# Kernel tuning notes

Measured on AMD Instinct MI355X. Metric: run time of the kernel, lower is better.

## Reference

```python
import jax, jax.numpy as jnp
import numpy as np

EPS = 1e-5

def _add_self_loops(edge_index, n):
    loop = jnp.arange(n, dtype=edge_index.dtype)
    return jnp.concatenate([edge_index, jnp.stack([loop, loop])], axis=1)

def _gcn_norm(row, col, n, dtype):
    # degree of target nodes (with self loops, unit edge weights)
    deg = jax.ops.segment_sum(jnp.ones(row.shape[0], dtype=dtype), col, num_segments=n)
    dinv = jnp.where(deg > 0, deg ** -0.5, 0.0).astype(dtype)
    return dinv[row] * dinv[col]  # [E]

def _propagate(xw, row, col, ew, n):
    # gather -> scale -> scatter-add
    msgs = ew[:, None] * xw[row]          # [E, C]
    return jax.ops.segment_sum(msgs, col, num_segments=n)  # [N, C]

def _batchnorm(x, gamma, beta):
    mu = jnp.mean(x, axis=0)
    var = jnp.var(x, axis=0)
    return (x - mu) * jax.lax.rsqrt(var + EPS) * gamma + beta

def setup_inputs() -> dict:
    key = jax.random.key(0)
    ks = jax.random.split(key, 10)
    N, C_in, C_h, C_out, E = 50000, 128, 128, 1, 600000
    x = jax.random.normal(ks[0], (N, C_in), dtype=jnp.float32)
    edge_index = jax.random.randint(ks[1], (2, E), 0, N, dtype=jnp.int64)
    s = 1.0 / np.sqrt(C_in)
    return {
        "x": x,
        "edge_index": edge_index,
        "gcn_w": jax.random.uniform(ks[2], (C_in, C_h), jnp.float32, -s, s),
        "gcn_b": jnp.zeros((C_h,), jnp.float32),
        "bn1_g": jnp.ones((C_h,), jnp.float32),
        "bn1_b": jnp.zeros((C_h,), jnp.float32),
        "dcn_w": jax.random.uniform(ks[3], (C_h, C_h), jnp.float32, -s, s),
        "dcn_b": jnp.zeros((C_h,), jnp.float32),
        "bn3_g": jnp.ones((C_h,), jnp.float32),
        "bn3_b": jnp.zeros((C_h,), jnp.float32),
        "out_w": jax.random.uniform(ks[4], (2 * C_h, C_out), jnp.float32, -s, s),
        "out_b": jnp.zeros((C_out,), jnp.float32),
    }

def reference(x, edge_index, gcn_w, gcn_b, bn1_g, bn1_b, dcn_w, dcn_b, bn3_g, bn3_b, out_w, out_b):
    n = x.shape[0]
    ei = _add_self_loops(edge_index, n)
    row, col = ei[0], ei[1]
    ew = _gcn_norm(row, col, n, x.dtype)

    # GCNConv: lin -> normalized aggregate -> bias
    h = _propagate(x @ gcn_w, row, col, ew, n) + gcn_b
    h = _batchnorm(h, bn1_g, bn1_b)

    # DegGNNConv: lin -> normalized aggregate -> elementwise gate with input -> bias
    out = _propagate(h @ dcn_w, row, col, ew, n)
    out = out * h + dcn_b
    out = _batchnorm(out, bn3_g, bn3_b)
    # dropout is identity in eval mode

    xc = jnp.concatenate([h, out], axis=-1)  # [N, 2*C_h]
    return xc @ out_w + out_b
```

## Files before the change

### kernel.cpp

```cpp
#include <hip/hip_runtime.h>
#include <hip/hip_bf16.h>
#include <cstdint>


typedef __attribute__((ext_vector_type(8))) short bf16x8;
typedef __attribute__((ext_vector_type(4))) float f32x4;

__device__ __forceinline__ ushort f2bf(float f) {
    union { float f; unsigned u; } c; c.f = f;
    unsigned u = c.u;
    return (ushort)((u + 0x7fffu + ((u >> 16) & 1u)) >> 16);
}
__device__ __forceinline__ unsigned pack2bf(float a, float b) {
    return (unsigned)f2bf(a) | ((unsigned)f2bf(b) << 16);
}
__device__ __forceinline__ float bflo(unsigned u) {
    union { unsigned i; float f; } c; c.i = u << 16; return c.f;
}
__device__ __forceinline__ float bfhi(unsigned u) {
    union { unsigned i; float f; } c; c.i = u & 0xffff0000u; return c.f;
}

__global__ void zero_kernel(uint4* __restrict__ p, int nwords) {
    int i = blockIdx.x * blockDim.x + threadIdx.x;
    if (i < nwords) p[i] = (uint4){0u, 0u, 0u, 0u};
}

__global__ void convert_kernel(const void* __restrict__ ei, int E,
                               int* __restrict__ count) {
    const int* e32 = (const int*)ei;
    bool is64 = ((e32[1] | e32[3] | e32[5] | e32[7]) == 0);
    int stride = gridDim.x * blockDim.x;
    for (int e = blockIdx.x * blockDim.x + threadIdx.x; e < E; e += stride) {
        int c = is64 ? (int)((const long long*)ei)[E + e] : e32[E + e];
        atomicAdd(&count[c], 1);
    }
}

__global__ __launch_bounds__(256) void bsum_kernel(const int* __restrict__ count,
                                                   int* __restrict__ bsum, int n) {
    int t = threadIdx.x;
    int i0 = blockIdx.x * 1024 + t * 4;
    int s = 0;
    if (i0 + 4 <= n) {
        int4 v = *(const int4*)&count[i0];
        s = v.x + v.y + v.z + v.w;
    } else {
        for (int i = i0; i < n; i++) s += count[i];
    }
    __shared__ int ls[256];
    ls[t] = s;
    __syncthreads();
    for (int off = 128; off > 0; off >>= 1) {
        if (t < off) ls[t] += ls[t + off];
        __syncthreads();
    }
    if (t == 0) bsum[blockIdx.x] = ls[0];
}

__global__ void scanb_kernel(int* __restrict__ bsum, int nb) {
    __shared__ int sm[1024];
    int t = threadIdx.x;
    int v = (t < nb) ? bsum[t] : 0;
    sm[t] = v;
    __syncthreads();
    for (int off = 1; off < 1024; off <<= 1) {
        int a = (t >= off) ? sm[t - off] : 0;
        __syncthreads();
        sm[t] += a;
        __syncthreads();
    }
    if (t < nb) bsum[t] = sm[t] - v;
}

__global__ __launch_bounds__(256) void emit_kernel(const int* __restrict__ count,
                                                   const int* __restrict__ bbase,
                                                   int* __restrict__ base, int n) {
    int t = threadIdx.x;
    int i0 = blockIdx.x * 1024 + t * 4;
    int v[4];
    int s = 0;
    if (i0 + 4 <= n) {
        int4 q = *(const int4*)&count[i0];
        v[0] = q.x; v[1] = q.y; v[2] = q.z; v[3] = q.w;
        s = v[0] + v[1] + v[2] + v[3];
    } else {
        #pragma unroll
        for (int k = 0; k < 4; k++) {
            int i = i0 + k;
            v[k] = (i < n) ? count[i] : 0;
            s += v[k];
        }
    }
    __shared__ int sm[256];
    sm[t] = s;
    __syncthreads();
    for (int off = 1; off < 256; off <<= 1) {
        int a = (t >= off) ? sm[t - off] : 0;
        __syncthreads();
        sm[t] += a;
        __syncthreads();
    }
    int run = bbase[blockIdx.x] + sm[t] - s;
    #pragma unroll
    for (int k = 0; k < 4; k++) {
        int i = i0 + k;
        if (i < n) {
            base[i] = run;
            run += v[k];
        }
    }
}

__global__ void scatter_kernel(const void* __restrict__ ei, int E,
                               const int* __restrict__ base, int* __restrict__ cursor,
                               const int* __restrict__ count,
                               unsigned* __restrict__ esrc) {
    const int* e32 = (const int*)ei;
    bool is64 = ((e32[1] | e32[3] | e32[5] | e32[7]) == 0);
    int stride = gridDim.x * blockDim.x;
    for (int e = blockIdx.x * blockDim.x + threadIdx.x; e < E; e += stride) {
        int r, c;
        if (is64) {
            r = (int)((const long long*)ei)[e];
            c = (int)((const long long*)ei)[E + e];
        } else {
            r = e32[e];
            c = e32[E + e];
        }
        int pos = base[c] + atomicAdd(&cursor[c], 1);
        unsigned deg = (unsigned)count[r];
        esrc[pos] = (deg << 24) | ((unsigned)r << 6);
    }
}

__global__ void wtrans_kernel(const float* __restrict__ W1, ushort* __restrict__ WT1,
                              const float* __restrict__ W2, ushort* __restrict__ WT2) {
    int b = blockIdx.x;
    const float* W = (b < 64) ? W1 : W2;
    ushort* WT = (b < 64) ? WT1 : WT2;
    int t = (b & 63) * 256 + threadIdx.x;
    int c = t >> 7, k = t & 127;
    WT[t] = f2bf(W[k * 128 + c]);
}

__global__ __launch_bounds__(256) void gemm_mfma_kernel(const float* __restrict__ Xf,
                                                        const ushort* __restrict__ Xb,
                                                        const ushort* __restrict__ WT,
                                                        const float* __restrict__ ab,
                                                        ushort* __restrict__ Ybf, int n) {
    __shared__ ushort Wl[128 * 136];
    int t = threadIdx.x;
    for (int idx = t * 8; idx < 128 * 128; idx += 256 * 8) {
        int c = idx >> 7;
        int k = idx & 127;
        *(uint4*)&Wl[c * 136 + k] = *(const uint4*)&WT[idx];
    }
    __syncthreads();

    int wid = t >> 6;
    int lane = t & 63;
    int m0 = blockIdx.x * 64 + wid * 16;
    if (m0 >= n) return;
    int row = m0 + (lane & 15);
    int rc = row < n ? row : n - 1;
    int kg = (lane >> 4) * 8;

    f32x4 acc[8];
    #pragma unroll
    for (int i = 0; i < 8; i++) acc[i] = (f32x4){0.f, 0.f, 0.f, 0.f};

    #pragma unroll
    for (int ks = 0; ks < 4; ks++) {
        int k0 = ks * 32 + kg;
        bf16x8 a;
        if (Xb) {
            uint4 q = *(const uint4*)&Xb[(size_t)rc * 128 + k0];
            float f0 = bflo(q.x), f1 = bfhi(q.x), f2 = bflo(q.y), f3 = bfhi(q.y);
            float f4 = bflo(q.z), f5 = bfhi(q.z), f6 = bflo(q.w), f7 = bfhi(q.w);
            float4 alo = *(const float4*)&ab[k0];
            float4 ahi = *(const float4*)&ab[k0 + 4];
            float4 blo = *(const float4*)&ab[128 + k0];
            float4 bhi = *(const float4*)&ab[128 + k0 + 4];
            a[0] = (short)f2bf(alo.x * f0 + blo.x);
            a[1] = (short)f2bf(alo.y * f1 + blo.y);
            a[2] = (short)f2bf(alo.z * f2 + blo.z);
            a[3] = (short)f2bf(alo.w * f3 + blo.w);
            a[4] = (short)f2bf(ahi.x * f4 + bhi.x);
            a[5] = (short)f2bf(ahi.y * f5 + bhi.y);
            a[6] = (short)f2bf(ahi.z * f6 + bhi.z);
            a[7] = (short)f2bf(ahi.w * f7 + bhi.w);
        } else {
            const float* xr = &Xf[(size_t)rc * 128];
            float4 lo = *(const float4*)&xr[k0];
            float4 hi = *(const float4*)&xr[k0 + 4];
            a[0] = (short)f2bf(lo.x); a[1] = (short)f2bf(lo.y);
            a[2] = (short)f2bf(lo.z); a[3] = (short)f2bf(lo.w);
            a[4] = (short)f2bf(hi.x); a[5] = (short)f2bf(hi.y);
            a[6] = (short)f2bf(hi.z); a[7] = (short)f2bf(hi.w);
        }
        #pragma unroll
        for (int nt = 0; nt < 8; nt++) {
            int c = nt * 16 + (lane & 15);
            bf16x8 b = *(bf16x8*)&Wl[c * 136 + k0];
            acc[nt] = __builtin_amdgcn_mfma_f32_16x16x32_bf16(a, b, acc[nt], 0, 0, 0);
        }
    }

    int ro = m0 + (lane >> 4) * 4;
    int co = lane & 15;
    #pragma unroll
    for (int nt = 0; nt < 8; nt++) {
        #pragma unroll
        for (int i = 0; i < 4; i++) {
            int r = ro + i;
            if (r < n) Ybf[(size_t)r * 128 + nt * 16 + co] = f2bf(acc[nt][i]);
        }
    }
}

__global__ __launch_bounds__(256) void prop_kernel(const unsigned* __restrict__ XWb,
                            const int* __restrict__ base,
                            const int* __restrict__ count, const unsigned* __restrict__ esrc,
                            const unsigned* __restrict__ B1bf, const float* __restrict__ ab1,
                            unsigned* __restrict__ outbf,
                            float* __restrict__ psum, float* __restrict__ psq,
                            int n, int gate) {
    int wave = (int)((blockIdx.x * blockDim.x + threadIdx.x) >> 6);
    int lane = threadIdx.x & 63;
    int wid = threadIdx.x >> 6;
    float vx = 0.f, vy = 0.f;
    if (wave < n) {
        int b = base[wave];
        int cnt = count[wave];
        float din = rsqrtf((float)(cnt + 1));
        float accx = 0.f, accy = 0.f;
        unsigned vs = XWb[(size_t)wave * 64 + lane];
        int i = 0;
        for (; i + 8 <= cnt; i += 8) {
            unsigned p[8], v[8];
            #pragma unroll
            for (int j = 0; j < 8; j++) p[j] = esrc[b + i + j];
            #pragma unroll
            for (int j = 0; j < 8; j++)
                v[j] = XWb[(size_t)(p[j] & 0xFFFFFFu) + lane];
            #pragma unroll
            for (int j = 0; j < 8; j++) {
                float w = rsqrtf((float)((p[j] >> 24) + 1));
                accx += w * bflo(v[j]);
                accy += w * bfhi(v[j]);
            }
        }
        for (; i + 4 <= cnt; i += 4) {
            unsigned p[4], v[4];
            #pragma unroll
            for (int j = 0; j < 4; j++) p[j] = esrc[b + i + j];
            #pragma unroll
            for (int j = 0; j < 4; j++)
                v[j] = XWb[(size_t)(p[j] & 0xFFFFFFu) + lane];
            #pragma unroll
            for (int j = 0; j < 4; j++) {
                float w = rsqrtf((float)((p[j] >> 24) + 1));
                accx += w * bflo(v[j]);
                accy += w * bfhi(v[j]);
            }
        }
        for (; i < cnt; i++) {
            unsigned p = esrc[b + i];
            unsigned v = XWb[(size_t)(p & 0xFFFFFFu) + lane];
            float w = rsqrtf((float)((p >> 24) + 1));
            accx += w * bflo(v);
            accy += w * bfhi(v);
        }
        accx = din * (accx + din * bflo(vs));
        accy = din * (accy + din * bfhi(vs));
        if (gate) {
            int c0 = 2 * lane;
            unsigned b1 = B1bf[(size_t)wave * 64 + lane];
            float h0 = ab1[c0] * bflo(b1) + ab1[128 + c0];
            float h1 = ab1[c0 + 1] * bfhi(b1) + ab1[128 + c0 + 1];
            vx = accx * h0;
            vy = accy * h1;
        } else {
            vx = accx;
            vy = accy;
        }
        outbf[(size_t)wave * 64 + lane] = pack2bf(vx, vy);
    }
    __shared__ float4 sm[4][64];
    float4 st; st.x = vx; st.y = vx * vx; st.z = vy; st.w = vy * vy;
    sm[wid][lane] = st;
    __syncthreads();
    if (threadIdx.x < 64) {
        float4 a0 = sm[0][lane], a1 = sm[1][lane], a2 = sm[2][lane], a3 = sm[3][lane];
        float s0 = a0.x + a1.x + a2.x + a3.x;
        float q0 = a0.y + a1.y + a2.y + a3.y;
        float s1 = a0.z + a1.z + a2.z + a3.z;
        float q1 = a0.w + a1.w + a2.w + a3.w;
        int slot = (blockIdx.x & 63) * 128;
        int c0 = 2 * lane;
        atomicAdd(&psum[slot + c0], s0);
        atomicAdd(&psq[slot + c0], q0);
        atomicAdd(&psum[slot + c0 + 1], s1);
        atomicAdd(&psq[slot + c0 + 1], q1);
    }
}

__global__ void reduce_ab_kernel(const float* __restrict__ psum, const float* __restrict__ psq,
                                 const float* __restrict__ g, const float* __restrict__ beta,
                                 float* __restrict__ ab, int n) {
    int c = threadIdx.x;
    float s = 0.f, s2 = 0.f;
    for (int r = 0; r < 64; r++) {
        s += psum[r * 128 + c];
        s2 += psq[r * 128 + c];
    }
    float invn = 1.f / (float)n;
    float mu = s * invn;
    float var = s2 * invn - mu * mu;
    float a = g[c] * rsqrtf(var + 1e-5f);
    ab[c] = a;
    ab[128 + c] = beta[c] - mu * a;
}

__global__ void final_kernel(const unsigned* __restrict__ B1bf, const unsigned* __restrict__ B2bf,
                             const float* __restrict__ ab1, const float* __restrict__ ab3,
                             const float* __restrict__ ow, const float* __restrict__ ob,
                             float* __restrict__ out, int n) {
    int wave = (int)((blockIdx.x * blockDim.x + threadIdx.x) >> 6);
    int lane = threadIdx.x & 63;
    if (wave >= n) return;
    int c0 = 2 * lane, c1 = c0 + 1;
    unsigned b1 = B1bf[(size_t)wave * 64 + lane];
    unsigned b2 = B2bf[(size_t)wave * 64 + lane];
    float h0 = ab1[c0] * bflo(b1) + ab1[128 + c0];
    float h1 = ab1[c1] * bfhi(b1) + ab1[128 + c1];
    float o0 = ab3[c0] * bflo(b2) + ab3[128 + c0];
    float o1 = ab3[c1] * bfhi(b2) + ab3[128 + c1];
    float partial = h0 * ow[c0] + h1 * ow[c1] + o0 * ow[128 + c0] + o1 * ow[128 + c1];
    #pragma unroll
    for (int off = 32; off > 0; off >>= 1) partial += __shfl_down(partial, off);
    if (lane == 0) out[wave] = partial + ob[0];
}

extern "C" void kernel_launch(void* const* d_in, const int* in_sizes, int n_in,
                              void* d_out, int out_size, void* d_ws, size_t ws_size,
                              hipStream_t stream) {
    const float* x     = (const float*)d_in[0];
    const void*  ei    = d_in[1];
    const float* gcn_w = (const float*)d_in[2];
    const float* bn1_g = (const float*)d_in[4];
    const float* bn1_b = (const float*)d_in[5];
    const float* dcn_w = (const float*)d_in[6];
    const float* bn3_g = (const float*)d_in[8];
    const float* bn3_b = (const float*)d_in[9];
    const float* out_w = (const float*)d_in[10];
    const float* out_b = (const float*)d_in[11];
    float* out = (float*)d_out;

    int N = in_sizes[0] / 128;
    int E = in_sizes[1] / 2;
    size_t N128 = (size_t)N * 128;

    ushort* Abf   = (ushort*)d_ws;
    ushort* B1bf  = Abf + N128;
    ushort* B2bf  = B1bf + N128;
    unsigned* esrc = (unsigned*)(B2bf + N128);
    int*   base  = (int*)(esrc + E);
    int*   bsum  = base + N;
    ushort* WT1  = (ushort*)(bsum + 1024);
    ushort* WT2  = WT1 + 16384;
    float* ab1   = (float*)(WT2 + 16384);
    float* ab3   = ab1 + 256;
    int*   count  = (int*)(ab3 + 256);
    int*   cursor = count + N;
    float* psum1  = (float*)(cursor + N);
    float* psq1   = psum1 + 8192;
    float* psum3  = psq1 + 8192;
    float* psq3   = psum3 + 8192;

    size_t zero_bytes = (size_t)((char*)(psq3 + 8192) - (char*)count);
    int zwords = (int)(zero_bytes / 16);
    zero_kernel<<<(zwords + 255) / 256, 256, 0, stream>>>((uint4*)count, zwords);

    int egrid = (E + 255) / 256;
    if (egrid > 2048) egrid = 2048;
    int pgrid = (N + 3) / 4;
    int nb = (N + 1023) / 1024;
    int ggrid = (N + 63) / 64;

    convert_kernel<<<egrid, 256, 0, stream>>>(ei, E, count);
    bsum_kernel<<<nb, 256, 0, stream>>>(count, bsum, N);
    scanb_kernel<<<1, 1024, 0, stream>>>(bsum, nb);
    emit_kernel<<<nb, 256, 0, stream>>>(count, bsum, base, N);
    scatter_kernel<<<egrid, 256, 0, stream>>>(ei, E, base, cursor, count, esrc);
    wtrans_kernel<<<128, 256, 0, stream>>>(gcn_w, WT1, dcn_w, WT2);

    gemm_mfma_kernel<<<ggrid, 256, 0, stream>>>(x, nullptr, WT1, nullptr, Abf, N);
    prop_kernel<<<pgrid, 256, 0, stream>>>((const unsigned*)Abf, base, count, esrc,
                                           nullptr, nullptr, (unsigned*)B1bf,
                                           psum1, psq1, N, 0);
    reduce_ab_kernel<<<1, 128, 0, stream>>>(psum1, psq1, bn1_g, bn1_b, ab1, N);

    gemm_mfma_kernel<<<ggrid, 256, 0, stream>>>(nullptr, B1bf, WT2, ab1, Abf, N);
    prop_kernel<<<pgrid, 256, 0, stream>>>((const unsigned*)Abf, base, count, esrc,
                                           (const unsigned*)B1bf, ab1, (unsigned*)B2bf,
                                           psum3, psq3, N, 1);
    reduce_ab_kernel<<<1, 128, 0, stream>>>(psum3, psq3, bn3_g, bn3_b, ab3, N);

    final_kernel<<<pgrid, 256, 0, stream>>>((const unsigned*)B1bf, (const unsigned*)B2bf,
                                            ab1, ab3, out_w, out_b, out, N);
}
```

Before: 199.2 us.

## Map four nodes per wave with 16-byte gathers in propagation kernel

The propagation kernel now assigns each 16-lane quarter-wave to one node, so every lane loads a uint4 (8 bf16 channels) per neighbor instead of one 32-bit word per lane. This cuts the number of gather instructions and spreads the load over more in-flight nodes. Batchnorm partial sums are reduced with cross-quarter shuffles before the shared-memory pass. In exchange, quarter-waves with different degrees diverge inside one wave, and the tail loop pads to multiples of four with clamped, zero-weighted loads.

```diff
diff --git a/kernel.cpp b/kernel.cpp
--- a/kernel.cpp
+++ b/kernel.cpp
@@ -219,90 +219,112 @@
     }
 }
 
-__global__ __launch_bounds__(256) void prop_kernel(const unsigned* __restrict__ XWb,
+__global__ __launch_bounds__(256) void prop_kernel(const uint4* __restrict__ XW4,
                             const int* __restrict__ base,
                             const int* __restrict__ count, const unsigned* __restrict__ esrc,
-                            const unsigned* __restrict__ B1bf, const float* __restrict__ ab1,
-                            unsigned* __restrict__ outbf,
+                            const uint4* __restrict__ B1q, const float* __restrict__ ab1,
+                            uint4* __restrict__ outq,
                             float* __restrict__ psum, float* __restrict__ psq,
                             int n, int gate) {
-    int wave = (int)((blockIdx.x * blockDim.x + threadIdx.x) >> 6);
+    int wave4 = (int)((blockIdx.x * blockDim.x + threadIdx.x) >> 6);
     int lane = threadIdx.x & 63;
     int wid = threadIdx.x >> 6;
-    float vx = 0.f, vy = 0.f;
-    if (wave < n) {
-        int b = base[wave];
-        int cnt = count[wave];
-        float din = rsqrtf((float)(cnt + 1));
-        float accx = 0.f, accy = 0.f;
-        unsigned vs = XWb[(size_t)wave * 64 + lane];
-        int i = 0;
-        for (; i + 8 <= cnt; i += 8) {
-            unsigned p[8], v[8];
-            #pragma unroll
-            for (int j = 0; j < 8; j++) p[j] = esrc[b + i + j];
-            #pragma unroll
-            for (int j = 0; j < 8; j++)
-                v[j] = XWb[(size_t)(p[j] & 0xFFFFFFu) + lane];
-            #pragma unroll
-            for (int j = 0; j < 8; j++) {
-                float w = rsqrtf((float)((p[j] >> 24) + 1));
-                accx += w * bflo(v[j]);
-                accy += w * bfhi(v[j]);
-            }
-        }
-        for (; i + 4 <= cnt; i += 4) {
-            unsigned p[4], v[4];
-            #pragma unroll
-            for (int j = 0; j < 4; j++) p[j] = esrc[b + i + j];
-            #pragma unroll
-            for (int j = 0; j < 4; j++)
-                v[j] = XWb[(size_t)(p[j] & 0xFFFFFFu) + lane];
-            #pragma unroll
-            for (int j = 0; j < 4; j++) {
-                float w = rsqrtf((float)((p[j] >> 24) + 1));
-                accx += w * bflo(v[j]);
-                accy += w * bfhi(v[j]);
-            }
-        }
-        for (; i < cnt; i++) {
-            unsigned p = esrc[b + i];
-            unsigned v = XWb[(size_t)(p & 0xFFFFFFu) + lane];
-            float w = rsqrtf((float)((p >> 24) + 1));
-            accx += w * bflo(v);
-            accy += w * bfhi(v);
-        }
-        accx = din * (accx + din * bflo(vs));
-        accy = din * (accy + din * bfhi(vs));
-        if (gate) {
-            int c0 = 2 * lane;
-            unsigned b1 = B1bf[(size_t)wave * 64 + lane];
-            float h0 = ab1[c0] * bflo(b1) + ab1[128 + c0];
-            float h1 = ab1[c0 + 1] * bfhi(b1) + ab1[128 + c0 + 1];
-            vx = accx * h0;
-            vy = accy * h1;
-        } else {
-            vx = accx;
-            vy = accy;
-        }
-        outbf[(size_t)wave * 64 + lane] = pack2bf(vx, vy);
-    }
-    __shared__ float4 sm[4][64];
-    float4 st; st.x = vx; st.y = vx * vx; st.z = vy; st.w = vy * vy;
-    sm[wid][lane] = st;
+    int g = lane >> 4;
+    int p = lane & 15;
+    int node = wave4 * 4 + g;
+    bool valid = node < n;
+    int nc = valid ? node : n - 1;
+    int b = 0, cnt = 0;
+    if (valid) { b = base[node]; cnt = count[node]; }
+    float din = rsqrtf((float)(cnt + 1));
+
+    uint4 vs = XW4[(size_t)nc * 16 + p];
+
+    float ax[8];
+    #pragma unroll
+    for (int k = 0; k < 8; k++) ax[k] = 0.f;
+
+    for (int i = 0; i < cnt; i += 4) {
+        unsigned pj[4];
+        uint4 vj[4];
+        #pragma unroll
+        for (int j = 0; j < 4; j++) {
+            int e = i + j;
+            pj[j] = esrc[b + (e < cnt ? e : cnt - 1)];
+        }
+        #pragma unroll
+        for (int j = 0; j < 4; j++)
+            vj[j] = XW4[((pj[j] & 0xFFFFFFu) >> 2) + p];
+        #pragma unroll
+        for (int j = 0; j < 4; j++) {
+            float w = (i + j < cnt) ? rsqrtf((float)((pj[j] >> 24) + 1)) : 0.f;
+            ax[0] += w * bflo(vj[j].x); ax[1] += w * bfhi(vj[j].x);
+            ax[2] += w * bflo(vj[j].y); ax[3] += w * bfhi(vj[j].y);
+            ax[4] += w * bflo(vj[j].z); ax[5] += w * bfhi(vj[j].z);
+            ax[6] += w * bflo(vj[j].w); ax[7] += w * bfhi(vj[j].w);
+        }
+    }
+
+    float sv[8];
+    sv[0] = bflo(vs.x); sv[1] = bfhi(vs.x); sv[2] = bflo(vs.y); sv[3] = bfhi(vs.y);
+    sv[4] = bflo(vs.z); sv[5] = bfhi(vs.z); sv[6] = bflo(vs.w); sv[7] = bfhi(vs.w);
+    #pragma unroll
+    for (int k = 0; k < 8; k++) ax[k] = din * (ax[k] + din * sv[k]);
+
+    float vv[8];
+    if (gate) {
+        uint4 b1 = B1q[(size_t)nc * 16 + p];
+        float bv[8];
+        bv[0] = bflo(b1.x); bv[1] = bfhi(b1.x); bv[2] = bflo(b1.y); bv[3] = bfhi(b1.y);
+        bv[4] = bflo(b1.z); bv[5] = bfhi(b1.z); bv[6] = bflo(b1.w); bv[7] = bfhi(b1.w);
+        int c0 = p * 8;
+        #pragma unroll
+        for (int k = 0; k < 8; k++) {
+            float h = ab1[c0 + k] * bv[k] + ab1[128 + c0 + k];
+            vv[k] = ax[k] * h;
+        }
+    } else {
+        #pragma unroll
+        for (int k = 0; k < 8; k++) vv[k] = ax[k];
+    }
+
+    if (valid) {
+        uint4 o;
+        o.x = pack2bf(vv[0], vv[1]);
+        o.y = pack2bf(vv[2], vv[3]);
+        o.z = pack2bf(vv[4], vv[5]);
+        o.w = pack2bf(vv[6], vv[7]);
+        outq[(size_t)node * 16 + p] = o;
+    } else {
+        #pragma unroll
+        for (int k = 0; k < 8; k++) vv[k] = 0.f;
+    }
+
+    float ss[8], qq[8];
+    #pragma unroll
+    for (int k = 0; k < 8; k++) { ss[k] = vv[k]; qq[k] = vv[k] * vv[k]; }
+    #pragma unroll
+    for (int k = 0; k < 8; k++) {
+        ss[k] += __shfl_xor(ss[k], 16); qq[k] += __shfl_xor(qq[k], 16);
+        ss[k] += __shfl_xor(ss[k], 32); qq[k] += __shfl_xor(qq[k], 32);
+    }
+    __shared__ float sm_s[4][128], sm_q[4][128];
+    if (g == 0) {
+        int c0 = p * 8;
+        #pragma unroll
+        for (int k = 0; k < 8; k++) {
+            sm_s[wid][c0 + k] = ss[k];
+            sm_q[wid][c0 + k] = qq[k];
+        }
+    }
     __syncthreads();
-    if (threadIdx.x < 64) {
-        float4 a0 = sm[0][lane], a1 = sm[1][lane], a2 = sm[2][lane], a3 = sm[3][lane];
-        float s0 = a0.x + a1.x + a2.x + a3.x;
-        float q0 = a0.y + a1.y + a2.y + a3.y;
-        float s1 = a0.z + a1.z + a2.z + a3.z;
-        float q1 = a0.w + a1.w + a2.w + a3.w;
+    if (threadIdx.x < 128) {
+        int c = threadIdx.x;
+        float s = sm_s[0][c] + sm_s[1][c] + sm_s[2][c] + sm_s[3][c];
+        float q2 = sm_q[0][c] + sm_q[1][c] + sm_q[2][c] + sm_q[3][c];
         int slot = (blockIdx.x & 63) * 128;
-        int c0 = 2 * lane;
-        atomicAdd(&psum[slot + c0], s0);
-        atomicAdd(&psq[slot + c0], q0);
-        atomicAdd(&psum[slot + c0 + 1], s1);
-        atomicAdd(&psq[slot + c0 + 1], q1);
+        atomicAdd(&psum[slot + c], s);
+        atomicAdd(&psq[slot + c], q2);
     }
 }
 
@@ -385,9 +407,10 @@
 
     int egrid = (E + 255) / 256;
     if (egrid > 2048) egrid = 2048;
-    int pgrid = (N + 3) / 4;
     int nb = (N + 1023) / 1024;
     int ggrid = (N + 63) / 64;
+    int pgrid = (N + 15) / 16;
+    int fgrid = (N + 3) / 4;
 
     convert_kernel<<<egrid, 256, 0, stream>>>(ei, E, count);
     bsum_kernel<<<nb, 256, 0, stream>>>(count, bsum, N);
@@ -397,17 +420,17 @@
     wtrans_kernel<<<128, 256, 0, stream>>>(gcn_w, WT1, dcn_w, WT2);
 
     gemm_mfma_kernel<<<ggrid, 256, 0, stream>>>(x, nullptr, WT1, nullptr, Abf, N);
-    prop_kernel<<<pgrid, 256, 0, stream>>>((const unsigned*)Abf, base, count, esrc,
-                                           nullptr, nullptr, (unsigned*)B1bf,
+    prop_kernel<<<pgrid, 256, 0, stream>>>((const uint4*)Abf, base, count, esrc,
+                                           nullptr, nullptr, (uint4*)B1bf,
                                            psum1, psq1, N, 0);
     reduce_ab_kernel<<<1, 128, 0, stream>>>(psum1, psq1, bn1_g, bn1_b, ab1, N);
 
     gemm_mfma_kernel<<<ggrid, 256, 0, stream>>>(nullptr, B1bf, WT2, ab1, Abf, N);
-    prop_kernel<<<pgrid, 256, 0, stream>>>((const unsigned*)Abf, base, count, esrc,
-                                           (const unsigned*)B1bf, ab1, (unsigned*)B2bf,
+    prop_kernel<<<pgrid, 256, 0, stream>>>((const uint4*)Abf, base, count, esrc,
+                                           (const uint4*)B1bf, ab1, (uint4*)B2bf,
                                            psum3, psq3, N, 1);
     reduce_ab_kernel<<<1, 128, 0, stream>>>(psum3, psq3, bn3_g, bn3_b, ab3, N);
 
-    final_kernel<<<pgrid, 256, 0, stream>>>((const unsigned*)B1bf, (const unsigned*)B2bf,
+    final_kernel<<<fgrid, 256, 0, stream>>>((const unsigned*)B1bf, (const unsigned*)B2bf,
                                             ab1, ab3, out_w, out_b, out, N);
 }
```

After: 172.2 us. 13.5% less time.
